# Kernel tuning notes

Measured on AMD Instinct MI355X. Metric: run time of the kernel, lower is better.

The kernel has to match this reference:

```python
import jax, jax.numpy as jnp
import numpy as np

A = 5          # angRes
C = 128        # channels
SPA = 2 * C    # spa_dim
NH = 8         # num_heads
KW = 11        # mask_field[1]


def setup_inputs() -> dict:
    key = jax.random.key(0)
    ks = jax.random.split(key, 12)
    s = 0.05
    return {
        "buffer": jax.random.normal(ks[0], (2, C, A * A, 32, 32), jnp.float32),
        "Win": jax.random.normal(ks[1], (SPA, C), jnp.float32) * s,
        "ln_w": jnp.ones((SPA,), jnp.float32),
        "ln_b": jnp.zeros((SPA,), jnp.float32),
        "in_proj": jax.random.normal(ks[2], (3 * SPA, SPA), jnp.float32) * s,
        "attn_out_w": jax.random.normal(ks[3], (SPA, SPA), jnp.float32) * s,
        "ffn_ln_w": jnp.ones((SPA,), jnp.float32),
        "ffn_ln_b": jnp.zeros((SPA,), jnp.float32),
        "ff1": jax.random.normal(ks[4], (2 * SPA, SPA), jnp.float32) * s,
        "ff2": jax.random.normal(ks[5], (SPA, 2 * SPA), jnp.float32) * s,
        "Wout": jax.random.normal(ks[6], (C, SPA), jnp.float32) * s,
        "conv_w": jax.random.normal(ks[7], (C, C, 1, 3, 3), jnp.float32) * s,
    }


def layer_norm(x, w, b, eps=1e-5):
    mu = x.mean(-1, keepdims=True)
    var = ((x - mu) ** 2).mean(-1, keepdims=True)
    return (x - mu) * jax.lax.rsqrt(var + eps) * w + b


def gen_mask(h, w, k_h, k_w):
    # additive mask over flattened (h*w) x (h*w) grid, local window k_h x k_w
    i = jnp.arange(h)
    j = jnp.arange(w)
    mh = (i[None, :] >= i[:, None] - k_h // 2) & (i[None, :] < i[:, None] + (k_h - k_h // 2))
    mw = (j[None, :] >= j[:, None] - k_w // 2) & (j[None, :] < j[:, None] + (k_w - k_w // 2))
    allowed = (mh[:, None, :, None] & mw[None, :, None, :]).reshape(h * w, h * w)
    return jnp.where(allowed, 0.0, -jnp.inf)


def basic_trans(x, Win, ln_w, ln_b, in_proj, attn_out_w,
                ffn_ln_w, ffn_ln_b, ff1, ff2, Wout):
    b, c, n, v, w = x.shape
    mask = gen_mask(v, w, 2 * A, KW)                       # (L, L)
    # 'b c n v w -> (v w) (b n) c'
    tok = x.transpose(3, 4, 0, 2, 1).reshape(v * w, b * n, c)
    tok = tok @ Win.T                                       # (L, B, E)
    tn = layer_norm(tok, ln_w, ln_b)
    L, B, E = tok.shape
    hd = E // NH
    Wq, Wk, Wv = jnp.split(in_proj, 3, axis=0)
    q = (tn @ Wq.T).reshape(L, B, NH, hd)
    k = (tn @ Wk.T).reshape(L, B, NH, hd)
    vv = (tok @ Wv.T).reshape(L, B, NH, hd)                 # value = un-normed tok
    scores = jnp.einsum('lbhd,mbhd->bhlm', q, k) / np.float32(np.sqrt(hd))
    scores = scores + mask[None, None]
    attn = jax.nn.softmax(scores, axis=-1)
    o = jnp.einsum('bhlm,mbhd->lbhd', attn, vv).reshape(L, B, E)
    tok = o @ attn_out_w.T + tok
    ff = layer_norm(tok, ffn_ln_w, ffn_ln_b)
    ff = jax.nn.relu(ff @ ff1.T) @ ff2.T
    tok = ff + tok
    tok = tok @ Wout.T                                      # (L, B, c)
    # '(v w) (b n) c -> b c n v w'
    return tok.reshape(v, w, b, n, c).transpose(2, 4, 3, 0, 1)


def reference(buffer, Win, ln_w, ln_b, in_proj, attn_out_w,
              ffn_ln_w, ffn_ln_b, ff1, ff2, Wout, conv_w):
    a = A
    b, c, uv, h, w = buffer.shape
    bt = lambda z: basic_trans(z, Win, ln_w, ln_b, in_proj, attn_out_w,
                               ffn_ln_w, ffn_ln_b, ff1, ff2, Wout)
    conv = lambda z: jax.lax.conv_general_dilated(
        z, conv_w, (1, 1, 1), ((0, 0), (1, 1), (1, 1)),
        dimension_numbers=('NCDHW', 'OIDHW', 'NCDHW'))

    # pass 1: 'b c (u v) h w -> b c (v w) u h'
    x = buffer.reshape(b, c, a, a, h, w).transpose(0, 1, 3, 5, 2, 4).reshape(b, c, a * w, a, h)
    x = bt(x)
    x = x.reshape(b, c, a, w, a, h).transpose(0, 1, 4, 2, 5, 3).reshape(b, c, a * a, h, w)
    x = conv(x) + buffer
    sc2 = x
    # pass 2: 'b c (u v) h w -> b c (u h) v w'
    y = x.reshape(b, c, a, a, h, w).transpose(0, 1, 2, 4, 3, 5).reshape(b, c, a * h, a, w)
    y = bt(y)
    y = y.reshape(b, c, a, h, a, w).transpose(0, 1, 2, 4, 3, 5).reshape(b, c, a * a, h, w)
    return conv(y) + sc2
```

## Files before the change

kernel.cpp:

```cpp
#include <hip/hip_runtime.h>
#include <math.h>
#include <stdint.h>

typedef __attribute__((ext_vector_type(8))) short bf16x8;
typedef __attribute__((ext_vector_type(4))) float f32x4;

static __device__ __forceinline__ unsigned short f2bf(float f) {
    unsigned u = __builtin_bit_cast(unsigned, f);
    unsigned r = u + 0x7fffu + ((u >> 16) & 1u);
    return (unsigned short)(r >> 16);
}
static __device__ __forceinline__ float bf2f(unsigned short h) {
    return __builtin_bit_cast(float, ((unsigned)h) << 16);
}
static __device__ __forceinline__ void gload_lds16(const void* g, void* l) {
    __builtin_amdgcn_global_load_lds((const __attribute__((address_space(1))) unsigned int*)g,
                                     (__attribute__((address_space(3))) unsigned int*)l, 16, 0, 0);
}

__global__ __launch_bounds__(256) void gather1(const float* __restrict__ src,
                                               unsigned short* __restrict__ x0, int W, int bb0) {
    int cct = blockIdx.x & 3, y = blockIdx.x >> 2;
    int n = blockIdx.y; int u = n / 5, v = n % 5;
    int lb = blockIdx.z, bb = bb0 + lb;
    __shared__ float tile[32][33];
    int tx = threadIdx.x & 31, tg = threadIdx.x >> 5;
    const float* s = src + (((size_t)(bb * 128 + cct * 32) * 25 + n) * 32 + y) * 32;
    #pragma unroll
    for (int i = 0; i < 4; i++) {
        int cl = tg + 8 * i;
        tile[cl][tx] = s[(size_t)cl * 25600 + tx];
    }
    __syncthreads();
    unsigned short* d = x0 + ((size_t)(u * 32 + y) * W + lb * 160 + v * 32) * 128 + cct * 32;
    #pragma unroll
    for (int i = 0; i < 4; i++) {
        int xx = tg + 8 * i;
        d[(size_t)xx * 128 + tx] = f2bf(tile[tx][xx]);
    }
}

__global__ __launch_bounds__(256) void gather2(const float* __restrict__ src,
                                               unsigned short* __restrict__ x0, int W, int bb0) {
    int cct = blockIdx.x & 3, x = blockIdx.x >> 2;
    int n = blockIdx.y; int u = n / 5, v = n % 5;
    int lb = blockIdx.z, bb = bb0 + lb;
    __shared__ float tile[32][33];
    int tx = threadIdx.x & 31, tg = threadIdx.x >> 5;
    const float* s = src + (((size_t)(bb * 128 + cct * 32) * 25 + n) * 32) * 32 + x;
    #pragma unroll
    for (int i = 0; i < 4; i++) {
        int cl = tg + 8 * i;
        tile[cl][tx] = s[(size_t)cl * 25600 + tx * 32];
    }
    __syncthreads();
    unsigned short* d = x0 + ((size_t)(v * 32 + x) * W + lb * 160 + u * 32) * 128 + cct * 32;
    #pragma unroll
    for (int i = 0; i < 4; i++) {
        int yy = tg + 8 * i;
        d[(size_t)yy * 128 + tx] = f2bf(tile[tx][yy]);
    }
}

__global__ __launch_bounds__(256) void repack_w(const float* __restrict__ cw,
                                                unsigned short* __restrict__ wb) {
    int g = blockIdx.x * 256 + threadIdx.x;
    int co = g / 1152;
    int rem = g - co * 1152;
    int ci = rem / 9, tap = rem - ci * 9;
    wb[((size_t)tap * 128 + co) * 128 + ci] = f2bf(cw[g]);
}

__global__ __launch_bounds__(256) void conv_weights(const float* __restrict__ Win,
                                                    const float* __restrict__ in_proj,
                                                    const float* __restrict__ attn_out_w,
                                                    const float* __restrict__ ff1,
                                                    const float* __restrict__ ff2,
                                                    const float* __restrict__ Wout,
                                                    unsigned short* __restrict__ wg) {
    int g = blockIdx.x * 256 + threadIdx.x;
    float v;
    if      (g < 32768)  v = Win[g];
    else if (g < 229376) v = in_proj[g - 32768];
    else if (g < 294912) v = attn_out_w[g - 229376];
    else if (g < 425984) v = ff1[g - 294912];
    else if (g < 557056) v = ff2[g - 425984];
    else                 v = Wout[g - 557056];
    wg[g] = f2bf(v);
}

__global__ __launch_bounds__(256) void ln_bf16(const unsigned short* __restrict__ in,
                                               unsigned short* __restrict__ out,
                                               const float* __restrict__ w, const float* __restrict__ b) {
    int tok = blockIdx.x * 4 + (threadIdx.x >> 6);
    int lane = threadIdx.x & 63;
    ushort4 h4 = ((const ushort4*)(in + (size_t)tok * 256))[lane];
    float vx = bf2f(h4.x), vy = bf2f(h4.y), vz = bf2f(h4.z), vw = bf2f(h4.w);
    float s = vx + vy + vz + vw;
    #pragma unroll
    for (int off = 32; off > 0; off >>= 1) s += __shfl_xor(s, off);
    float mu = s * (1.0f / 256.0f);
    float dx = vx - mu, dy = vy - mu, dz = vz - mu, dw = vw - mu;
    float vs = dx * dx + dy * dy + dz * dz + dw * dw;
    #pragma unroll
    for (int off = 32; off > 0; off >>= 1) vs += __shfl_xor(vs, off);
    float inv = rsqrtf(vs * (1.0f / 256.0f) + 1e-5f);
    float4 wv = ((const float4*)w)[lane];
    float4 bv = ((const float4*)b)[lane];
    ushort4 o4;
    o4.x = f2bf(dx * inv * wv.x + bv.x);
    o4.y = f2bf(dy * inv * wv.y + bv.y);
    o4.z = f2bf(dz * inv * wv.z + bv.z);
    o4.w = f2bf(dw * inv * wv.w + bv.w);
    *(ushort4*)(out + (size_t)tok * 256 + lane * 4) = o4;
}

static __device__ __forceinline__ void xcd_remap(int& bxi, int& byi) {
    int d = blockIdx.x + gridDim.x * blockIdx.y;
    int s = d & 7;
    unsigned j = (unsigned)(d >> 3);
    unsigned ny = gridDim.y;
    int gm8 = (int)(gridDim.x >> 3);
    bxi = s * gm8 + (int)(j / ny);
    byi = (int)(j % ny);
}

static __device__ __forceinline__ void gemm_core64(const unsigned short* __restrict__ X,
                                                   const unsigned short* __restrict__ Wt,
                                                   int bm, int bnrow, int K,
                                                   unsigned short (&As)[2][64 * 32],
                                                   unsigned short (&Bs)[2][64 * 32],
                                                   f32x4 (&acc)[2][2]) {
    const int tid = threadIdx.x;
    const int lane = tid & 63, w = tid >> 6;
    const int wm = (w >> 1) * 32, wn = (w & 1) * 32;
    const int lr = lane & 15, lq = lane >> 4;
    #pragma unroll
    for (int m = 0; m < 2; m++)
        #pragma unroll
        for (int n = 0; n < 2; n++)
            acc[m][n] = (f32x4){0.f, 0.f, 0.f, 0.f};

    const int srow = tid >> 2, sslot = tid & 3;
    const int ssl = sslot ^ ((srow >> 1) & 3);
    auto STAGE = [&](int bsel, int k0) {
        gload_lds16(X  + (size_t)(bm + srow) * K + k0 + ssl * 8,
                    &As[bsel][tid * 8]);
        gload_lds16(Wt + (size_t)(bnrow + srow) * K + k0 + ssl * 8,
                    &Bs[bsel][tid * 8]);
    };

    const int nt = K >> 5;
    STAGE(0, 0);
    __syncthreads();
    int cur = 0;
    for (int t = 0; t < nt; ++t) {
        if (t + 1 < nt) STAGE(cur ^ 1, (t + 1) << 5);
        const char* Ab = (const char*)As[cur];
        const char* Bb = (const char*)Bs[cur];
        bf16x8 af[2], bf[2];
        #pragma unroll
        for (int m = 0; m < 2; m++) {
            int row = wm + m * 16 + lr;
            af[m] = *(const bf16x8*)(Ab + row * 64 + ((lq * 16) ^ (((row >> 1) & 3) << 4)));
        }
        #pragma unroll
        for (int n = 0; n < 2; n++) {
            int row = wn + n * 16 + lr;
            bf[n] = *(const bf16x8*)(Bb + row * 64 + ((lq * 16) ^ (((row >> 1) & 3) << 4)));
        }
        #pragma unroll
        for (int m = 0; m < 2; m++)
            #pragma unroll
            for (int n = 0; n < 2; n++)
                acc[m][n] = __builtin_amdgcn_mfma_f32_16x16x32_bf16(af[m], bf[n], acc[m][n], 0, 0, 0);
        if (t + 1 < nt) __syncthreads();
        cur ^= 1;
    }
}

__global__ __launch_bounds__(256) void gemm_bf16(const unsigned short* __restrict__ X,
                                                 const unsigned short* __restrict__ Wt,
                                                 unsigned short* __restrict__ Yb,
                                                 const unsigned short* __restrict__ Rb,
                                                 int N, int K, int relu, int spass, int W) {
    __shared__ unsigned short As[2][64 * 32];
    __shared__ unsigned short Bs[2][64 * 32];
    int bxi, byi;
    xcd_remap(bxi, byi);
    const int bm = bxi * 64, bn = byi * 64;
    f32x4 acc[2][2];
    gemm_core64(X, Wt, bm, bn, K, As, Bs, acc);

    const int lane = threadIdx.x & 63, w = threadIdx.x >> 6;
    const int wm = (w >> 1) * 32, wn = (w & 1) * 32;
    const int lr = lane & 15, lq = lane >> 4;
    #pragma unroll
    for (int m = 0; m < 2; m++) {
        #pragma unroll
        for (int r = 0; r < 4; r++) {
            int row = bm + wm + m * 16 + lq * 4 + r;
            size_t base;
            if (spass == 0) {
                base = (size_t)row * N;
            } else {
                int l = row / W, c = row - l * W;
                int lb = (c >= 160) ? 1 : 0, sp = c - lb * 160;
                int sl_, pix;
                if (spass == 1) { int u = l >> 5, y = l & 31, v = sp >> 5, x = sp & 31;
                                  sl_ = lb * 25 + u * 5 + v; pix = y * 32 + x; }
                else            { int v = l >> 5, x = l & 31, u = sp >> 5, y = sp & 31;
                                  sl_ = lb * 25 + u * 5 + v; pix = y * 32 + x; }
                base = ((size_t)sl_ * 1024 + pix) * 128;
            }
            #pragma unroll
            for (int n = 0; n < 2; n++) {
                int col = bn + wn + n * 16 + lr;
                float val = acc[m][n][r];
                if (Rb) val += bf2f(Rb[(size_t)row * N + col]);
                if (relu) val = fmaxf(val, 0.0f);
                Yb[base + col] = f2bf(val);
            }
        }
    }
}

__global__ __launch_bounds__(256) void gemm_qkv(const unsigned short* __restrict__ tn,
                                                const unsigned short* __restrict__ tok,
                                                const unsigned short* __restrict__ Wqkv,
                                                unsigned short* __restrict__ QK,
                                                unsigned short* __restrict__ V) {
    __shared__ unsigned short As[2][64 * 32];
    __shared__ unsigned short Bs[2][64 * 32];
    int bxi, by;
    xcd_remap(bxi, by);
    const int bm = bxi * 64;
    const unsigned short* X = (by < 8) ? tn : tok;
    f32x4 acc[2][2];
    gemm_core64(X, Wqkv, bm, by * 64, 256, As, Bs, acc);

    unsigned short* Yb = (by < 8) ? QK : V;
    const int N = (by < 8) ? 512 : 256;
    const int bn = (by < 8) ? by * 64 : (by - 8) * 64;
    const int lane = threadIdx.x & 63, w = threadIdx.x >> 6;
    const int wm = (w >> 1) * 32, wn = (w & 1) * 32;
    const int lr = lane & 15, lq = lane >> 4;
    #pragma unroll
    for (int m = 0; m < 2; m++) {
        #pragma unroll
        for (int r = 0; r < 4; r++) {
            int row = bm + wm + m * 16 + lq * 4 + r;
            #pragma unroll
            for (int n = 0; n < 2; n++) {
                int col = bn + wn + n * 16 + lr;
                Yb[(size_t)row * N + col] = f2bf(acc[m][n][r]);
            }
        }
    }
}

__global__ __launch_bounds__(256) void vtrans(const unsigned short* __restrict__ vtok,
                                              unsigned short* __restrict__ vt, int W) {
    const int col = blockIdx.x, h = blockIdx.y;
    __shared__ unsigned short t[160][34];
    const int tid = threadIdx.x;
    for (int i = tid; i < 160 * 16; i += 256) {
        int l = i >> 4, dp = i & 15;
        unsigned v = *(const unsigned*)(vtok + ((size_t)l * W + col) * 256 + h * 32 + dp * 2);
        *(unsigned*)&t[l][dp * 2] = v;
    }
    __syncthreads();
    unsigned short* dst = vt + (((size_t)h * W + col) * 32) * 160;
    for (int i = tid; i < 32 * 160; i += 256) {
        int d = i / 160, l = i - d * 160;
        dst[i] = t[l][d];
    }
}

__global__ __launch_bounds__(64) void attn_mfma(const unsigned short* __restrict__ qk,
                                                const unsigned short* __restrict__ vt,
                                                unsigned short* __restrict__ o, int W) {
    const int col = blockIdx.x;
    const int h = blockIdx.y;
    const int lane = threadIdx.x;
    const int lr = lane & 15, lq = lane >> 4;
    __shared__ __align__(16) unsigned short P_lds[16][168];

    bf16x8 kf[10];
    #pragma unroll
    for (int m = 0; m < 10; m++) {
        size_t t = (size_t)(m * 16 + lr) * W + col;
        kf[m] = *(const bf16x8*)(qk + t * 512 + 256 + h * 32 + lq * 8);
    }
    const unsigned short* vbase = vt + (((size_t)h * W + col) * 32) * 160;
    bf16x8 vf[2][5];
    #pragma unroll
    for (int md = 0; md < 2; md++)
        #pragma unroll
        for (int c = 0; c < 5; c++)
            vf[md][c] = *(const bf16x8*)(vbase + (size_t)(md * 16 + lr) * 160 + c * 32 + lq * 8);

    const float scale = 0.17677669529663687f;
    for (int n = 0; n < 10; n++) {
        const int q = n * 16 + lr;
        bf16x8 qf = *(const bf16x8*)(qk + ((size_t)q * W + col) * 512 + h * 32 + lq * 8);
        f32x4 p[10];
        #pragma unroll
        for (int m = 0; m < 10; m++)
            p[m] = __builtin_amdgcn_mfma_f32_16x16x32_bf16(kf[m], qf, (f32x4){0.f,0.f,0.f,0.f}, 0, 0, 0);
        const int b = lq * 4 - ((n & 1) * 16 + lr);
        float mx = -1e30f;
        #pragma unroll
        for (int m = 0; m < 10; m++) {
            #pragma unroll
            for (int r = 0; r < 4; r++) {
                int dd = b + (m & 1) * 16 + r;
                float s = ((unsigned)(dd + 5) <= 10u) ? p[m][r] : -1e30f;
                p[m][r] = s;
                mx = fmaxf(mx, s);
            }
        }
        mx = fmaxf(mx, __shfl_xor(mx, 16));
        mx = fmaxf(mx, __shfl_xor(mx, 32));
        float sum = 0.f;
        #pragma unroll
        for (int m = 0; m < 10; m++) {
            #pragma unroll
            for (int r = 0; r < 4; r++) {
                float e = __expf((p[m][r] - mx) * scale);
                p[m][r] = e;
                sum += e;
            }
        }
        sum += __shfl_xor(sum, 16);
        sum += __shfl_xor(sum, 32);
        #pragma unroll
        for (int m = 0; m < 10; m++) {
            ushort4 pk;
            pk.x = f2bf(p[m][0]); pk.y = f2bf(p[m][1]);
            pk.z = f2bf(p[m][2]); pk.w = f2bf(p[m][3]);
            *(ushort4*)&P_lds[lr][m * 16 + lq * 4] = pk;
        }
        f32x4 oa0 = (f32x4){0.f,0.f,0.f,0.f}, oa1 = (f32x4){0.f,0.f,0.f,0.f};
        #pragma unroll
        for (int c = 0; c < 5; c++) {
            bf16x8 pf = *(const bf16x8*)&P_lds[lr][c * 32 + lq * 8];
            oa0 = __builtin_amdgcn_mfma_f32_16x16x32_bf16(vf[0][c], pf, oa0, 0, 0, 0);
            oa1 = __builtin_amdgcn_mfma_f32_16x16x32_bf16(vf[1][c], pf, oa1, 0, 0, 0);
        }
        const float inv = 1.0f / sum;
        unsigned short* op = o + ((size_t)q * W + col) * 256 + h * 32;
        ushort4 s0, s1;
        s0.x = f2bf(oa0[0] * inv); s0.y = f2bf(oa0[1] * inv);
        s0.z = f2bf(oa0[2] * inv); s0.w = f2bf(oa0[3] * inv);
        s1.x = f2bf(oa1[0] * inv); s1.y = f2bf(oa1[1] * inv);
        s1.z = f2bf(oa1[2] * inv); s1.w = f2bf(oa1[3] * inv);
        *(ushort4*)(op + lq * 4)      = s0;
        *(ushort4*)(op + 16 + lq * 4) = s1;
    }
}

__global__ __launch_bounds__(256) void conv_mfma(const unsigned short* __restrict__ xp,
                                                 const unsigned short* __restrict__ wb,
                                                 const float* __restrict__ res,
                                                 float* __restrict__ out, int bb0) {
    const int ptile = blockIdx.x;
    const int slice = blockIdx.y;
    const int lb = slice / 25, n = slice % 25;
    const int bb = bb0 + lb;
    const int y0 = ptile * 4;
    __shared__ unsigned short As[128 * 64];
    __shared__ unsigned short Bs[128 * 64];
    const int tid = threadIdx.x;
    const int lane = tid & 63, w = tid >> 6;
    const int wm = (w >> 1) * 64;
    const int wn = (w & 1) * 64;
    const int lr = lane & 15, lq = lane >> 4;
    const unsigned short* xs = xp + (size_t)slice * 1024 * 128;
    f32x4 acc[4][4];
    #pragma unroll
    for (int m = 0; m < 4; m++)
        #pragma unroll
        for (int nn = 0; nn < 4; nn++)
            acc[m][nn] = (f32x4){0.f, 0.f, 0.f, 0.f};

    for (int tap = 0; tap < 9; tap++) {
        const int dy = tap / 3 - 1, dx = tap % 3 - 1;
        for (int c0 = 0; c0 < 128; c0 += 64) {
            #pragma unroll
            for (int i = 0; i < 4; i++) {
                int id = tid + 256 * i;
                int row = id >> 3, cg = id & 7;
                int py = y0 + (row >> 5) + dy;
                int px = (row & 31) + dx;
                uint4 v = {0u, 0u, 0u, 0u};
                if ((unsigned)py < 32u && (unsigned)px < 32u)
                    v = *(const uint4*)(xs + ((size_t)(py * 32 + px) * 128 + c0 + cg * 8));
                int boff = row * 128 + ((cg * 16) ^ ((row & 7) << 4));
                *(uint4*)((char*)As + boff) = v;
            }
            #pragma unroll
            for (int i = 0; i < 4; i++) {
                int id = tid + 256 * i;
                int row = id >> 3, cg = id & 7;
                uint4 v = *(const uint4*)(wb + (((size_t)tap * 128 + row) * 128 + c0 + cg * 8));
                int boff = row * 128 + ((cg * 16) ^ ((row & 7) << 4));
                *(uint4*)((char*)Bs + boff) = v;
            }
            __syncthreads();
            #pragma unroll
            for (int ks = 0; ks < 2; ks++) {
                bf16x8 wf[4], xf[4];
                #pragma unroll
                for (int m = 0; m < 4; m++) {
                    int row = wm + m * 16 + lr;
                    int boff = row * 128 + ((ks * 64 + lq * 16) ^ ((row & 7) << 4));
                    wf[m] = *(const bf16x8*)((const char*)Bs + boff);
                }
                #pragma unroll
                for (int nn = 0; nn < 4; nn++) {
                    int row = wn + nn * 16 + lr;
                    int boff = row * 128 + ((ks * 64 + lq * 16) ^ ((row & 7) << 4));
                    xf[nn] = *(const bf16x8*)((const char*)As + boff);
                }
                #pragma unroll
                for (int m = 0; m < 4; m++)
                    #pragma unroll
                    for (int nn = 0; nn < 4; nn++)
                        acc[m][nn] = __builtin_amdgcn_mfma_f32_16x16x32_bf16(wf[m], xf[nn], acc[m][nn], 0, 0, 0);
            }
            __syncthreads();
        }
    }
    #pragma unroll
    for (int m = 0; m < 4; m++) {
        int co0 = wm + m * 16 + lq * 4;
        #pragma unroll
        for (int r = 0; r < 4; r++) {
            size_t rowoff = (((size_t)(bb * 128 + co0 + r) * 25 + n) * 1024) + ptile * 128;
            #pragma unroll
            for (int nn = 0; nn < 4; nn++) {
                int pix = wn + nn * 16 + lr;
                out[rowoff + pix] = acc[m][nn][r] + res[rowoff + pix];
            }
        }
    }
}

extern "C" void kernel_launch(void* const* d_in, const int* in_sizes, int n_in,
                              void* d_out, int out_size, void* d_ws, size_t ws_size,
                              hipStream_t stream) {
    (void)in_sizes; (void)n_in; (void)out_size;
    const float* buffer     = (const float*)d_in[0];
    const float* Win        = (const float*)d_in[1];
    const float* ln_w       = (const float*)d_in[2];
    const float* ln_b       = (const float*)d_in[3];
    const float* in_proj    = (const float*)d_in[4];
    const float* attn_out_w = (const float*)d_in[5];
    const float* ffn_ln_w   = (const float*)d_in[6];
    const float* ffn_ln_b   = (const float*)d_in[7];
    const float* ff1        = (const float*)d_in[8];
    const float* ff2        = (const float*)d_in[9];
    const float* Wout       = (const float*)d_in[10];
    const float* conv_w     = (const float*)d_in[11];
    float* out = (float*)d_out;
    float* ws  = (float*)d_ws;

    const size_t need2 = ((size_t)51200 * 960 + 368640) * 4;
    int NBB = (ws_size >= need2) ? 2 : 1;
    const int W = NBB * 160;
    const size_t T = (size_t)NBB * 25600;

    unsigned short* x0b   = (unsigned short*)ws;
    unsigned short* Abf   = (unsigned short*)(ws + T * 64);
    unsigned short* tnb   = (unsigned short*)(ws + T * 192);
    float*          C     = ws + T * 320;
    unsigned short* QKtok = (unsigned short*)C;
    unsigned short* Vtok  = (unsigned short*)(C + T * 256);
    unsigned short* Vt    = (unsigned short*)(C + T * 384);
    unsigned short* hidb  = (unsigned short*)C;
    unsigned short* xp    = (unsigned short*)C;
    unsigned short* Db    = (unsigned short*)(ws + T * 832);
    unsigned short* wg    = (unsigned short*)(ws + T * 960);
    unsigned short* wb    = (unsigned short*)(ws + T * 960 + 294912);

    const unsigned short* Winb  = wg;
    const unsigned short* Wqkvb = wg + 32768;
    const unsigned short* Waob  = wg + 229376;
    const unsigned short* Wff1b = wg + 294912;
    const unsigned short* Wff2b = wg + 425984;
    const unsigned short* Woutb = wg + 557056;

    const int GM64 = (int)(T / 64);

    conv_weights<<<2304, 256, 0, stream>>>(Win, in_proj, attn_out_w, ff1, ff2, Wout, wg);
    repack_w<<<576, 256, 0, stream>>>(conv_w, wb);

    for (int pass = 0; pass < 2; pass++) {
        const float* src = (pass == 0) ? buffer : out;
        for (int bb0 = 0; bb0 < 2; bb0 += NBB) {
            if (pass == 0) gather1<<<dim3(128, 25, NBB), 256, 0, stream>>>(src, x0b, W, bb0);
            else           gather2<<<dim3(128, 25, NBB), 256, 0, stream>>>(src, x0b, W, bb0);

            gemm_bf16<<<dim3(GM64, 4), 256, 0, stream>>>(x0b, Winb, Abf, nullptr, 256, 128, 0, 0, W);
            ln_bf16<<<(int)(T / 4), 256, 0, stream>>>(Abf, tnb, ln_w, ln_b);
            gemm_qkv<<<dim3(GM64, 12), 256, 0, stream>>>(tnb, Abf, Wqkvb, QKtok, Vtok);
            vtrans<<<dim3(W, 8), 256, 0, stream>>>(Vtok, Vt, W);
            attn_mfma<<<dim3(W, 8), 64, 0, stream>>>(QKtok, Vt, Db, W);
            gemm_bf16<<<dim3(GM64, 4), 256, 0, stream>>>(Db, Waob, Abf, Abf, 256, 256, 0, 0, W);
            ln_bf16<<<(int)(T / 4), 256, 0, stream>>>(Abf, tnb, ffn_ln_w, ffn_ln_b);
            gemm_bf16<<<dim3(GM64, 8), 256, 0, stream>>>(tnb, Wff1b, hidb, nullptr, 512, 256, 1, 0, W);
            gemm_bf16<<<dim3(GM64, 4), 256, 0, stream>>>(hidb, Wff2b, Abf, Abf, 256, 512, 0, 0, W);
            gemm_bf16<<<dim3(GM64, 2), 256, 0, stream>>>(Abf, Woutb, xp, nullptr, 128, 256, 0, pass + 1, W);

            conv_mfma<<<dim3(8, NBB * 25), 256, 0, stream>>>(
                xp, wb, (pass == 0) ? buffer : (const float*)out, out, bb0);
        }
    }
}
```

Baseline: 593.2 us.

## Fuse FFN up-projection, ReLU and down-projection into one kernel

Replaces the two FFN GEMM launches with a single kernel. Each block of 64 tokens keeps its input rows in registers, computes 64-wide hidden chunks with ReLU into shared memory, and accumulates the second projection immediately. The residual add is applied at the end. This removes the global round trip of the 512-wide hidden activation and one launch. In exchange the grid is 4-8x smaller, there are more syncs per chunk, and weights are reloaded per block.

New measurement: 563.1 us. 1.05x faster.

```diff
diff --git a/kernel.cpp b/kernel.cpp
--- a/kernel.cpp
+++ b/kernel.cpp
@@ -257,6 +257,125 @@
             }
         }
     }
+}
+
+__global__ __launch_bounds__(256) void ffn_fused(const unsigned short* __restrict__ X,
+                                                 const unsigned short* __restrict__ W1,
+                                                 const unsigned short* __restrict__ W2,
+                                                 unsigned short* __restrict__ R) {
+    __shared__ unsigned short Wc[64 * 256];
+    __shared__ unsigned short Hs[64 * 64];
+    const int tid = threadIdx.x;
+    const int lane = tid & 63, w = tid >> 6;
+    const int lr = lane & 15, lq = lane >> 4;
+    const int wm = (w >> 1) * 32;
+    const int wn1 = (w & 1) * 32;
+    const int wn2 = (w & 1) * 128;
+    const int bm = blockIdx.x * 64;
+
+    bf16x8 xf[2][8];
+    #pragma unroll
+    for (int m = 0; m < 2; m++) {
+        const unsigned short* xr = X + (size_t)(bm + wm + m * 16 + lr) * 256 + lq * 8;
+        #pragma unroll
+        for (int ks = 0; ks < 8; ks++)
+            xf[m][ks] = *(const bf16x8*)(xr + ks * 32);
+    }
+
+    f32x4 acc_o[2][8];
+    #pragma unroll
+    for (int m = 0; m < 2; m++)
+        #pragma unroll
+        for (int nt = 0; nt < 8; nt++)
+            acc_o[m][nt] = (f32x4){0.f, 0.f, 0.f, 0.f};
+
+    for (int hk = 0; hk < 8; hk++) {
+        if (hk) __syncthreads();
+        #pragma unroll
+        for (int i = 0; i < 8; i++) {
+            int d = (w << 13) + (i << 10) + (lane << 4);
+            int h = d >> 9, s = (d >> 4) & 31;
+            int ss = s ^ (h & 7);
+            gload_lds16(W1 + (size_t)(hk * 64 + h) * 256 + ss * 8,
+                        (char*)Wc + (w << 13) + (i << 10));
+        }
+        __syncthreads();
+
+        f32x4 acc1[2][2];
+        #pragma unroll
+        for (int m = 0; m < 2; m++)
+            #pragma unroll
+            for (int n = 0; n < 2; n++)
+                acc1[m][n] = (f32x4){0.f, 0.f, 0.f, 0.f};
+        #pragma unroll
+        for (int ks = 0; ks < 8; ks++) {
+            bf16x8 bf[2];
+            #pragma unroll
+            for (int n = 0; n < 2; n++) {
+                int hrow = wn1 + n * 16 + lr;
+                int slot = ks * 4 + lq;
+                bf[n] = *(const bf16x8*)((const char*)Wc + hrow * 512 + ((slot ^ (hrow & 7)) << 4));
+            }
+            #pragma unroll
+            for (int m = 0; m < 2; m++)
+                #pragma unroll
+                for (int n = 0; n < 2; n++)
+                    acc1[m][n] = __builtin_amdgcn_mfma_f32_16x16x32_bf16(xf[m][ks], bf[n], acc1[m][n], 0, 0, 0);
+        }
+        #pragma unroll
+        for (int m = 0; m < 2; m++)
+            #pragma unroll
+            for (int n = 0; n < 2; n++)
+                #pragma unroll
+                for (int r = 0; r < 4; r++) {
+                    int trow = wm + m * 16 + lq * 4 + r;
+                    int hcol = wn1 + n * 16 + lr;
+                    *(unsigned short*)((char*)Hs + trow * 128 +
+                        (((hcol >> 3) ^ (trow & 7)) << 4) + (hcol & 7) * 2) =
+                        f2bf(fmaxf(acc1[m][n][r], 0.0f));
+                }
+        __syncthreads();
+
+        #pragma unroll
+        for (int i = 0; i < 8; i++) {
+            int d = (w << 13) + (i << 10) + (lane << 4);
+            int o = d >> 7, s = (d >> 4) & 7;
+            int ss = s ^ (o & 7);
+            gload_lds16(W2 + (size_t)o * 512 + hk * 64 + ss * 8,
+                        (char*)Wc + (w << 13) + (i << 10));
+        }
+        __syncthreads();
+
+        #pragma unroll
+        for (int ks = 0; ks < 2; ks++) {
+            int slot = ks * 4 + lq;
+            bf16x8 af2[2];
+            #pragma unroll
+            for (int m = 0; m < 2; m++) {
+                int trow = wm + m * 16 + lr;
+                af2[m] = *(const bf16x8*)((const char*)Hs + trow * 128 + ((slot ^ (trow & 7)) << 4));
+            }
+            #pragma unroll
+            for (int nt = 0; nt < 8; nt++) {
+                int orow = wn2 + nt * 16 + lr;
+                bf16x8 b2 = *(const bf16x8*)((const char*)Wc + orow * 128 + ((slot ^ (orow & 7)) << 4));
+                #pragma unroll
+                for (int m = 0; m < 2; m++)
+                    acc_o[m][nt] = __builtin_amdgcn_mfma_f32_16x16x32_bf16(af2[m], b2, acc_o[m][nt], 0, 0, 0);
+            }
+        }
+    }
+    #pragma unroll
+    for (int m = 0; m < 2; m++)
+        #pragma unroll
+        for (int nt = 0; nt < 8; nt++)
+            #pragma unroll
+            for (int r = 0; r < 4; r++) {
+                int row = bm + wm + m * 16 + lq * 4 + r;
+                int col = wn2 + nt * 16 + lr;
+                size_t off = (size_t)row * 256 + col;
+                R[off] = f2bf(acc_o[m][nt][r] + bf2f(R[off]));
+            }
 }
 
 __global__ __launch_bounds__(256) void vtrans(const unsigned short* __restrict__ vtok,
@@ -478,7 +597,6 @@
     unsigned short* QKtok = (unsigned short*)C;
     unsigned short* Vtok  = (unsigned short*)(C + T * 256);
     unsigned short* Vt    = (unsigned short*)(C + T * 384);
-    unsigned short* hidb  = (unsigned short*)C;
     unsigned short* xp    = (unsigned short*)C;
     unsigned short* Db    = (unsigned short*)(ws + T * 832);
     unsigned short* wg    = (unsigned short*)(ws + T * 960);
@@ -509,8 +627,7 @@
             attn_mfma<<<dim3(W, 8), 64, 0, stream>>>(QKtok, Vt, Db, W);
             gemm_bf16<<<dim3(GM64, 4), 256, 0, stream>>>(Db, Waob, Abf, Abf, 256, 256, 0, 0, W);
             ln_bf16<<<(int)(T / 4), 256, 0, stream>>>(Abf, tnb, ffn_ln_w, ffn_ln_b);
-            gemm_bf16<<<dim3(GM64, 8), 256, 0, stream>>>(tnb, Wff1b, hidb, nullptr, 512, 256, 1, 0, W);
-            gemm_bf16<<<dim3(GM64, 4), 256, 0, stream>>>(hidb, Wff2b, Abf, Abf, 256, 512, 0, 0, W);
+            ffn_fused<<<GM64, 256, 0, stream>>>(tnb, Wff1b, Wff2b, Abf);
             gemm_bf16<<<dim3(GM64, 2), 256, 0, stream>>>(Abf, Woutb, xp, nullptr, 128, 256, 0, pass + 1, W);
 
             conv_mfma<<<dim3(8, NBB * 25), 256, 0, stream>>>(
```
